# Optimization experiments

Hardware: AMD Instinct MI355X
Metric: run time of the kernel (lower is better)

Reference implementation:

```python
import jax, jax.numpy as jnp
import numpy as np

N, C, E, H = 10000, 128, 640000, 8


def setup_inputs() -> dict:
    key = jax.random.key(0)
    k1, k2, k3, k4, k5 = jax.random.split(key, 5)
    x = jax.random.normal(k1, (N, C), dtype=jnp.float32)
    edge_index = jax.random.randint(k2, (2, E), 0, N, dtype=jnp.int64)
    edge_attr = jax.random.uniform(k3, (E,), dtype=jnp.float32)
    W = jax.random.normal(k4, (2 * C, H), dtype=jnp.float32) * (1.0 / np.sqrt(2 * C))
    b = jax.random.normal(k5, (H,), dtype=jnp.float32) * 0.01
    return {"x": x, "edge_index": edge_index, "edge_attr": edge_attr, "W": W, "b": b}


def reference(x, edge_index, edge_attr, W, b):
    row, col = edge_index[0], edge_index[1]
    # Split W so we never materialize the concatenated [E, 2C] tensor:
    # cat([x[row], x[col]]) @ W == x[row] @ W[:C] + x[col] @ W[C:]
    Wr, Wc = W[:x.shape[1]], W[x.shape[1]:]
    logits = x[row] @ Wr + x[col] @ Wc + b          # [E, H]
    alpha = jax.nn.sigmoid(logits) * edge_attr[:, None]
    self_loop = (row == col)[:, None]                # [E, 1] -> broadcast over heads
    alpha = jnp.where(self_loop, jnp.ones((), dtype=alpha.dtype), alpha)
    return (alpha, edge_index)
```

## Files before the change

### kernel.cpp

```cpp
#include <hip/hip_runtime.h>

#define N_NODES  10000
#define C_DIM    128
#define H_DIM    8
#define YZ_TOTAL (N_NODES * H_DIM)

typedef _Float16 h2 __attribute__((ext_vector_type(2)));
typedef _Float16 h8 __attribute__((ext_vector_type(8)));

__global__ void __launch_bounds__(256)
precompute_yz(const float* __restrict__ x, const float* __restrict__ W,
              const float* __restrict__ b, _Float16* __restrict__ yzh) {
    const int t = blockIdx.x * blockDim.x + threadIdx.x;
    const int n = t >> 5;
    if (n >= N_NODES) return;
    const int w  = t & 31;
    const int s  = w >> 2;
    const int hp = w & 3;
    const int h0 = hp * 2;

    const float4* xr4 = (const float4*)(x + (size_t)n * C_DIM) + s * 4;
    float4 xv0 = xr4[0], xv1 = xr4[1], xv2 = xr4[2], xv3 = xr4[3];
    const float xk[16] = { xv0.x,xv0.y,xv0.z,xv0.w, xv1.x,xv1.y,xv1.z,xv1.w,
                           xv2.x,xv2.y,xv2.z,xv2.w, xv3.x,xv3.y,xv3.z,xv3.w };

    const int k0 = s * 16;
    const float* wr = W + (size_t)k0 * H_DIM + h0;
    const float* wc = W + (size_t)(C_DIM + k0) * H_DIM + h0;

    float ar0 = 0.f, ar1 = 0.f, ac0 = 0.f, ac1 = 0.f;
#pragma unroll
    for (int j = 0; j < 16; ++j) {
        float2 wr2 = *(const float2*)(wr + j * H_DIM);
        float2 wc2 = *(const float2*)(wc + j * H_DIM);
        ar0 = fmaf(xk[j], wr2.x, ar0);
        ar1 = fmaf(xk[j], wr2.y, ar1);
        ac0 = fmaf(xk[j], wc2.x, ac0);
        ac1 = fmaf(xk[j], wc2.y, ac1);
    }
#pragma unroll
    for (int m = 4; m <= 16; m <<= 1) {
        ar0 += __shfl_xor(ar0, m, 64);
        ar1 += __shfl_xor(ar1, m, 64);
        ac0 += __shfl_xor(ac0, m, 64);
        ac1 += __shfl_xor(ac1, m, 64);
    }
    if (s == 0) {
        float2 bb = *(const float2*)(b + h0);
        h2 yv = { (_Float16)(ar0 + bb.x), (_Float16)(ar1 + bb.y) };
        h2 zv = { (_Float16)ac0,          (_Float16)ac1 };
        *(h2*)(yzh + (size_t)n * H_DIM + h0)            = yv;
        *(h2*)(yzh + YZ_TOTAL + (size_t)n * H_DIM + h0) = zv;
    }
}

__device__ __forceinline__ float sigmoid_fast(float v) {
    return __builtin_amdgcn_rcpf(1.f + __expf(-v));
}

__global__ void edge_alpha(const int* __restrict__ ei,
                           const float* __restrict__ ea,
                           const _Float16* __restrict__ yzh,
                           float* __restrict__ out, int E) {
    const int e = blockIdx.x * blockDim.x + threadIdx.x;
    if (e >= E) return;
    int r = ei[e];
    int c = ei[E + e];
    float a = ea[e];

    h8 yv = *(const h8*)(yzh + (size_t)r * H_DIM);
    h8 zv = *(const h8*)(yzh + YZ_TOTAL + (size_t)c * H_DIM);

    const bool self = (r == c);
    float res[8];
#pragma unroll
    for (int h = 0; h < 8; ++h) {
        float v = (float)yv[h] + (float)zv[h];
        res[h] = self ? 1.f : sigmoid_fast(v) * a;
    }

    float4* op = (float4*)(out + (size_t)e * H_DIM);
    op[0] = make_float4(res[0], res[1], res[2], res[3]);
    op[1] = make_float4(res[4], res[5], res[6], res[7]);

    out[(size_t)E * H_DIM + e]     = (float)r;
    out[(size_t)E * H_DIM + E + e] = (float)c;
}

extern "C" void kernel_launch(void* const* d_in, const int* in_sizes, int n_in,
                              void* d_out, int out_size, void* d_ws, size_t ws_size,
                              hipStream_t stream) {
    const float* x  = (const float*)d_in[0];
    const int*   ei = (const int*)d_in[1];
    const float* ea = (const float*)d_in[2];
    const float* W  = (const float*)d_in[3];
    const float* b  = (const float*)d_in[4];
    float* out = (float*)d_out;
    _Float16* yzh = (_Float16*)d_ws;
    const int E = in_sizes[2];

    {
        const int total_threads = N_NODES * 32;
        const int grid = (total_threads + 255) / 256;
        hipLaunchKernelGGL(precompute_yz, dim3(grid), dim3(256), 0, stream,
                           x, W, b, yzh);
    }
    {
        const int grid = (E + 255) / 256;
        hipLaunchKernelGGL(edge_alpha, dim3(grid), dim3(256), 0, stream,
                           ei, ea, yzh, out, E);
    }
}
```

Before: 23.61 us.

## Move edge-index float conversion into the node-projection kernel's extra blocks

The int-to-float conversion of edge_index moves out of the edge kernel and into extra blocks of the first kernel. Those blocks use 16-byte vector loads and stores. The aim is to overlap this memory-bound copy with the small per-node projection, which alone leaves most of the GPU idle, and to lighten the edge kernel. The edge kernel still reads the indices for its gathers, so the index array is now read twice.

```diff
diff --git a/kernel.cpp b/kernel.cpp
--- a/kernel.cpp
+++ b/kernel.cpp
@@ -1,56 +1,74 @@
 #include <hip/hip_runtime.h>
 
-#define N_NODES  10000
-#define C_DIM    128
-#define H_DIM    8
-#define YZ_TOTAL (N_NODES * H_DIM)
+#define N_NODES   10000
+#define C_DIM     128
+#define H_DIM     8
+#define YZ_TOTAL  (N_NODES * H_DIM)
+#define YZ_BLOCKS ((N_NODES * 32) / 256)
 
 typedef _Float16 h2 __attribute__((ext_vector_type(2)));
 typedef _Float16 h8 __attribute__((ext_vector_type(8)));
 
 __global__ void __launch_bounds__(256)
-precompute_yz(const float* __restrict__ x, const float* __restrict__ W,
-              const float* __restrict__ b, _Float16* __restrict__ yzh) {
-    const int t = blockIdx.x * blockDim.x + threadIdx.x;
-    const int n = t >> 5;
-    if (n >= N_NODES) return;
-    const int w  = t & 31;
-    const int s  = w >> 2;
-    const int hp = w & 3;
-    const int h0 = hp * 2;
+k1_yz_and_index(const float* __restrict__ x, const float* __restrict__ W,
+                const float* __restrict__ b, const int* __restrict__ ei,
+                float* __restrict__ out, _Float16* __restrict__ yzh, int E) {
+    const int bid = blockIdx.x;
 
-    const float4* xr4 = (const float4*)(x + (size_t)n * C_DIM) + s * 4;
-    float4 xv0 = xr4[0], xv1 = xr4[1], xv2 = xr4[2], xv3 = xr4[3];
-    const float xk[16] = { xv0.x,xv0.y,xv0.z,xv0.w, xv1.x,xv1.y,xv1.z,xv1.w,
-                           xv2.x,xv2.y,xv2.z,xv2.w, xv3.x,xv3.y,xv3.z,xv3.w };
+    if (bid < YZ_BLOCKS) {
+        const int t = bid * 256 + threadIdx.x;
+        const int n = t >> 5;
+        if (n >= N_NODES) return;
+        const int w  = t & 31;
+        const int s  = w >> 2;
+        const int hp = w & 3;
+        const int h0 = hp * 2;
 
-    const int k0 = s * 16;
-    const float* wr = W + (size_t)k0 * H_DIM + h0;
-    const float* wc = W + (size_t)(C_DIM + k0) * H_DIM + h0;
+        const float4* xr4 = (const float4*)(x + (size_t)n * C_DIM) + s * 4;
+        float4 xv0 = xr4[0], xv1 = xr4[1], xv2 = xr4[2], xv3 = xr4[3];
+        const float xk[16] = { xv0.x,xv0.y,xv0.z,xv0.w, xv1.x,xv1.y,xv1.z,xv1.w,
+                               xv2.x,xv2.y,xv2.z,xv2.w, xv3.x,xv3.y,xv3.z,xv3.w };
 
-    float ar0 = 0.f, ar1 = 0.f, ac0 = 0.f, ac1 = 0.f;
+        const int k0 = s * 16;
+        const float* wr = W + (size_t)k0 * H_DIM + h0;
+        const float* wc = W + (size_t)(C_DIM + k0) * H_DIM + h0;
+
+        float ar0 = 0.f, ar1 = 0.f, ac0 = 0.f, ac1 = 0.f;
 #pragma unroll
-    for (int j = 0; j < 16; ++j) {
-        float2 wr2 = *(const float2*)(wr + j * H_DIM);
-        float2 wc2 = *(const float2*)(wc + j * H_DIM);
-        ar0 = fmaf(xk[j], wr2.x, ar0);
-        ar1 = fmaf(xk[j], wr2.y, ar1);
-        ac0 = fmaf(xk[j], wc2.x, ac0);
-        ac1 = fmaf(xk[j], wc2.y, ac1);
-    }
+        for (int j = 0; j < 16; ++j) {
+            float2 wr2 = *(const float2*)(wr + j * H_DIM);
+            float2 wc2 = *(const float2*)(wc + j * H_DIM);
+            ar0 = fmaf(xk[j], wr2.x, ar0);
+            ar1 = fmaf(xk[j], wr2.y, ar1);
+            ac0 = fmaf(xk[j], wc2.x, ac0);
+            ac1 = fmaf(xk[j], wc2.y, ac1);
+        }
 #pragma unroll
-    for (int m = 4; m <= 16; m <<= 1) {
-        ar0 += __shfl_xor(ar0, m, 64);
-        ar1 += __shfl_xor(ar1, m, 64);
-        ac0 += __shfl_xor(ac0, m, 64);
-        ac1 += __shfl_xor(ac1, m, 64);
-    }
-    if (s == 0) {
-        float2 bb = *(const float2*)(b + h0);
-        h2 yv = { (_Float16)(ar0 + bb.x), (_Float16)(ar1 + bb.y) };
-        h2 zv = { (_Float16)ac0,          (_Float16)ac1 };
-        *(h2*)(yzh + (size_t)n * H_DIM + h0)            = yv;
-        *(h2*)(yzh + YZ_TOTAL + (size_t)n * H_DIM + h0) = zv;
+        for (int m = 4; m <= 16; m <<= 1) {
+            ar0 += __shfl_xor(ar0, m, 64);
+            ar1 += __shfl_xor(ar1, m, 64);
+            ac0 += __shfl_xor(ac0, m, 64);
+            ac1 += __shfl_xor(ac1, m, 64);
+        }
+        if (s == 0) {
+            float2 bb = *(const float2*)(b + h0);
+            h2 yv = { (_Float16)(ar0 + bb.x), (_Float16)(ar1 + bb.y) };
+            h2 zv = { (_Float16)ac0,          (_Float16)ac1 };
+            *(h2*)(yzh + (size_t)n * H_DIM + h0)            = yv;
+            *(h2*)(yzh + YZ_TOTAL + (size_t)n * H_DIM + h0) = zv;
+        }
+    } else {
+        const size_t ib = (size_t)E * H_DIM;
+        const int t = (bid - YZ_BLOCKS) * 256 + threadIdx.x;
+        const int i = t * 4;
+        const int total = 2 * E;
+        if (i + 3 < total) {
+            int4 v = *(const int4*)(ei + i);
+            *(float4*)(out + ib + i) =
+                make_float4((float)v.x, (float)v.y, (float)v.z, (float)v.w);
+        } else {
+            for (int j = i; j < total; ++j) out[ib + j] = (float)ei[j];
+        }
     }
 }
 
@@ -82,9 +100,6 @@
     float4* op = (float4*)(out + (size_t)e * H_DIM);
     op[0] = make_float4(res[0], res[1], res[2], res[3]);
     op[1] = make_float4(res[4], res[5], res[6], res[7]);
-
-    out[(size_t)E * H_DIM + e]     = (float)r;
-    out[(size_t)E * H_DIM + E + e] = (float)c;
 }
 
 extern "C" void kernel_launch(void* const* d_in, const int* in_sizes, int n_in,
@@ -100,10 +115,11 @@
     const int E = in_sizes[2];
 
     {
-        const int total_threads = N_NODES * 32;
-        const int grid = (total_threads + 255) / 256;
-        hipLaunchKernelGGL(precompute_yz, dim3(grid), dim3(256), 0, stream,
-                           x, W, b, yzh);
+        const int conv_threads = (2 * E + 3) / 4;
+        const int conv_blocks  = (conv_threads + 255) / 256;
+        const int grid = YZ_BLOCKS + conv_blocks;
+        hipLaunchKernelGGL(k1_yz_and_index, dim3(grid), dim3(256), 0, stream,
+                           x, W, b, ei, out, yzh, E);
     }
     {
         const int grid = (E + 255) / 256;
```

Measured after the change: 23.62 us. Within noise of the previous version (+0.0%).
